# Kernel tuning notes

Hardware: AMD Instinct MI355X
Metric: run time of the kernel (lower is better)

Reference implementation:

```python
import jax, jax.numpy as jnp
import numpy as np

N_NODES = 100000
N_EDGES = 1200000
D_FEAT = 64
THETA = (1.0, -0.8, 0.4, -0.1)  # polynomial coefficients, k = len(THETA)


def setup_inputs() -> dict:
    key = jax.random.key(0)
    k1, k2, k3 = jax.random.split(key, 3)
    feat = jax.random.normal(k1, (N_NODES, D_FEAT), dtype=jnp.float32)
    src = jax.random.randint(k2, (N_EDGES,), 0, N_NODES, dtype=jnp.int32)
    dst = jax.random.randint(k3, (N_EDGES,), 0, N_NODES, dtype=jnp.int32)
    return {"feat": feat, "src": src, "dst": dst}


def reference(feat, src, dst):
    # in-degrees: number of incoming edges per node (clamped to >= 1)
    deg = jax.ops.segment_sum(jnp.ones((N_EDGES,), feat.dtype), dst, num_segments=N_NODES)
    d_invsqrt = jnp.clip(deg, 1.0, None) ** -0.5  # [N]
    d = d_invsqrt[:, None]  # [N, 1]

    h = THETA[0] * feat
    for k in range(1, len(THETA)):
        # unnLaplacian: feat - D^{-1/2} A^T (D^{-1/2} feat)  (copy_u / sum over edges)
        msg = (feat * d)[src]                                   # [E, F] gather
        agg = jax.ops.segment_sum(msg, dst, num_segments=N_NODES)  # [N, F] scatter-add
        feat = feat - agg * d
        h = h + THETA[k] * feat
    return h
```

## Files before the change

### kernel.cpp

```cpp
#include <hip/hip_runtime.h>

#define D_FEAT 64
#define BSHIFT 8
#define MAXB 512
#define CHUNK 4096

typedef float nfloat4 __attribute__((ext_vector_type(4)));

__device__ inline unsigned short f2bf(float f) {
    unsigned u = __float_as_uint(f);
    unsigned r = u + 0x7fffu + ((u >> 16) & 1u);
    return (unsigned short)(r >> 16);
}
__device__ inline float bflo(unsigned w) { return __uint_as_float(w << 16); }
__device__ inline float bfhi(unsigned w) { return __uint_as_float(w & 0xffff0000u); }

__device__ inline void unpack8(uint4 u, float* v) {
    v[0] = bflo(u.x); v[1] = bfhi(u.x);
    v[2] = bflo(u.y); v[3] = bfhi(u.y);
    v[4] = bflo(u.z); v[5] = bfhi(u.z);
    v[6] = bflo(u.w); v[7] = bfhi(u.w);
}
__device__ inline uint4 pack8(const float* v) {
    uint4 u;
    u.x = (unsigned)f2bf(v[0]) | ((unsigned)f2bf(v[1]) << 16);
    u.y = (unsigned)f2bf(v[2]) | ((unsigned)f2bf(v[3]) << 16);
    u.z = (unsigned)f2bf(v[4]) | ((unsigned)f2bf(v[5]) << 16);
    u.w = (unsigned)f2bf(v[6]) | ((unsigned)f2bf(v[7]) << 16);
    return u;
}

__global__ void pre_kernel(const int* __restrict__ dst, int* __restrict__ mat,
                           const float4* __restrict__ f, uint4* __restrict__ fb,
                           int nE, int P, int nblk, int n8) {
    __shared__ int lh[MAXB];
    int b = blockIdx.x;
    if (b < nblk) {
        for (int i = threadIdx.x; i < P; i += blockDim.x) lh[i] = 0;
        __syncthreads();
        int s = b * CHUNK;
        int e1 = s + CHUNK; if (e1 > nE) e1 = nE;
        for (int e = s + threadIdx.x; e < e1; e += blockDim.x)
            atomicAdd(&lh[dst[e] >> BSHIFT], 1);
        __syncthreads();
        for (int i = threadIdx.x; i < P; i += blockDim.x)
            mat[i * nblk + b] = lh[i];
    } else {
        int i = (b - nblk) * 256 + threadIdx.x;
        if (i < n8) {
            float4 a = f[(size_t)i * 2];
            float4 c = f[(size_t)i * 2 + 1];
            float v[8] = {a.x, a.y, a.z, a.w, c.x, c.y, c.z, c.w};
            fb[i] = pack8(v);
        }
    }
}

__global__ void scan1_kernel(const int* __restrict__ in, int* __restrict__ out,
                             int* __restrict__ bsums, int n) {
    __shared__ int tmp[256];
    int tid = threadIdx.x;
    int i = blockIdx.x * 256 + tid;
    int v = (i < n) ? in[i] : 0;
    tmp[tid] = v;
    __syncthreads();
    for (int off = 1; off < 256; off <<= 1) {
        int t2 = 0;
        if (tid >= off) t2 = tmp[tid - off];
        __syncthreads();
        tmp[tid] += t2;
        __syncthreads();
    }
    if (i < n) out[i] = tmp[tid] - v;
    if (tid == 255) bsums[blockIdx.x] = tmp[255];
}

__global__ void scan2_kernel(int* __restrict__ bsums, int nb) {
    __shared__ int tmp[512];
    int tid = threadIdx.x;
    int v = (tid < nb) ? bsums[tid] : 0;
    tmp[tid] = v;
    __syncthreads();
    for (int off = 1; off < 512; off <<= 1) {
        int t2 = 0;
        if (tid >= off) t2 = tmp[tid - off];
        __syncthreads();
        tmp[tid] += t2;
        __syncthreads();
    }
    if (tid < nb) bsums[tid] = tmp[tid] - v;
}

__global__ void scan3add_kernel(int* __restrict__ matS, const int* __restrict__ bsums,
                                int* __restrict__ bucket_ptr, int n, int nblk,
                                int P, int nE) {
    int i = blockIdx.x * 256 + threadIdx.x;
    if (i < n) {
        int v = matS[i] + bsums[blockIdx.x];
        matS[i] = v;
        if (i % nblk == 0) bucket_ptr[i / nblk] = v;
    }
    if (i == 0) bucket_ptr[P] = nE;
}

__global__ void scatter_part_kernel(const int* __restrict__ src, const int* __restrict__ dst,
                                    const int* __restrict__ matS, unsigned* __restrict__ part,
                                    int nE, int P, int nblk) {
    __shared__ int cur[MAXB];
    for (int i = threadIdx.x; i < P; i += blockDim.x)
        cur[i] = matS[i * nblk + blockIdx.x];
    __syncthreads();
    int s = blockIdx.x * CHUNK;
    int e1 = s + CHUNK; if (e1 > nE) e1 = nE;
    for (int e = s + threadIdx.x; e < e1; e += blockDim.x) {
        int t = dst[e];
        int pos = atomicAdd(&cur[t >> BSHIFT], 1);
        part[pos] = ((unsigned)src[e] << 8) | (unsigned)(t & 255);
    }
}

__global__ void bucket_csr_kernel(const unsigned* __restrict__ part,
                                  const int* __restrict__ bucket_ptr,
                                  int* __restrict__ row_ptr, int* __restrict__ row_end,
                                  float* __restrict__ dv, int* __restrict__ esrc, int nN) {
    __shared__ int hist[256];
    __shared__ int cur[256];
    __shared__ int scanT[256];
    int b = blockIdx.x;
    int tid = threadIdx.x;
    int bp0 = bucket_ptr[b], bp1 = bucket_ptr[b + 1];
    hist[tid] = 0;
    __syncthreads();
    for (int e = bp0 + tid; e < bp1; e += 256)
        atomicAdd(&hist[part[e] & 255u], 1);
    __syncthreads();
    int v = hist[tid];
    scanT[tid] = v;
    __syncthreads();
    for (int off = 1; off < 256; off <<= 1) {
        int t2 = 0;
        if (tid >= off) t2 = scanT[tid - off];
        __syncthreads();
        scanT[tid] += t2;
        __syncthreads();
    }
    int startv = scanT[tid] - v;
    cur[tid] = startv;
    int node = (b << BSHIFT) + tid;
    if (node < nN) {
        float fc = (float)(v < 1 ? 1 : v);
        dv[node] = rsqrtf(fc);
        row_ptr[node] = bp0 + startv;
        row_end[node] = bp0 + startv + v;
    }
    __syncthreads();
    for (int e = bp0 + tid; e < bp1; e += 256) {
        unsigned p = part[e];
        int rank = atomicAdd(&cur[p & 255u], 1);
        esrc[bp0 + rank] = (int)(p >> 8);
    }
}

__global__ void poly_kernel(const uint4* __restrict__ fb_in, uint4* __restrict__ fb_out,
                            const int* __restrict__ row_ptr, const int* __restrict__ row_end,
                            const int* __restrict__ esrc, const float* __restrict__ d,
                            const uint4* __restrict__ fb0, const uint4* __restrict__ fb1,
                            float* __restrict__ h, int final_step, int nN) {
    int wave = (blockIdx.x * blockDim.x + threadIdx.x) >> 6;
    int lane = threadIdx.x & 63;
    int sub  = lane >> 3;
    int q    = lane & 7;
    int t    = wave * 8 + sub;
    bool valid = (t < nN);
    if (!valid) t = nN - 1;

    int r0 = row_ptr[t], r1 = row_end[t];
    if (!valid) r1 = r0;

    float acc[8];
#pragma unroll
    for (int c = 0; c < 8; ++c) acc[c] = 0.0f;

    int   sq = 0;
    float dq = 0.0f;
    if (r0 < r1) {
        int jc = r0 + q; if (jc > r1 - 1) jc = r1 - 1;
        sq = esrc[jc];
        dq = d[sq];
    }
    int j0 = r0;
    while (j0 < r1) {
        int jn = j0 + 8;
        int   sq_n = 0;
        float dq_n = 0.0f;
        if (jn < r1) {
            int jc = jn + q; if (jc > r1 - 1) jc = r1 - 1;
            sq_n = esrc[jc];
            dq_n = d[sq_n];
        }
        int m = r1 - j0; if (m > 8) m = 8;
#pragma unroll
        for (int u = 0; u < 4; ++u) {
            int bl = (sub << 3) + u;
            int   sb = __shfl(sq, bl, 64);
            float ds = __shfl(dq, bl, 64);
            ds = (u < m) ? ds : 0.0f;
            uint4 fv = fb_in[(size_t)sb * 8 + q];
            float v[8];
            unpack8(fv, v);
#pragma unroll
            for (int c = 0; c < 8; ++c) acc[c] = fmaf(v[c], ds, acc[c]);
        }
        if (m > 4) {
#pragma unroll
            for (int u = 4; u < 8; ++u) {
                int bl = (sub << 3) + u;
                int   sb = __shfl(sq, bl, 64);
                float ds = __shfl(dq, bl, 64);
                ds = (u < m) ? ds : 0.0f;
                uint4 fv = fb_in[(size_t)sb * 8 + q];
                float v[8];
                unpack8(fv, v);
#pragma unroll
                for (int c = 0; c < 8; ++c) acc[c] = fmaf(v[c], ds, acc[c]);
            }
        }
        sq = sq_n; dq = dq_n; j0 = jn;
    }

    if (!valid) return;
    size_t idx = (size_t)t * 8 + q;
    float dt = d[t];
    float fo[8];
    unpack8(fb_in[idx], fo);
    float fn[8];
#pragma unroll
    for (int c = 0; c < 8; ++c) fn[c] = fo[c] - acc[c] * dt;

    if (!final_step) {
        fb_out[idx] = pack8(fn);
    } else {
        float f1v[8];
        unpack8(fb1[idx], f1v);
        float f0v[8];
        unpack8(fb0[idx], f0v);
        float hv[8];
#pragma unroll
        for (int c = 0; c < 8; ++c)
            hv[c] = f0v[c] - 0.8f * f1v[c] + 0.4f * fo[c] - 0.1f * fn[c];
        nfloat4 h0 = {hv[0], hv[1], hv[2], hv[3]};
        nfloat4 h1 = {hv[4], hv[5], hv[6], hv[7]};
        nfloat4* hp = (nfloat4*)(h + (size_t)t * 64 + q * 8);
        __builtin_nontemporal_store(h0, hp);
        __builtin_nontemporal_store(h1, hp + 1);
    }
}

extern "C" void kernel_launch(void* const* d_in, const int* in_sizes, int n_in,
                              void* d_out, int out_size, void* d_ws, size_t ws_size,
                              hipStream_t stream) {
    const float* feat = (const float*)d_in[0];
    const int*   src  = (const int*)d_in[1];
    const int*   dst  = (const int*)d_in[2];
    float*       h    = (float*)d_out;

    const int nN = in_sizes[0] / D_FEAT;
    const int nE = in_sizes[1];

    const int P    = (nN + 255) >> 8;
    const int nblk = (nE + CHUNK - 1) / CHUNK;
    const int n    = P * nblk;
    const int nb   = (n + 255) / 256;

    auto align = [](size_t x) { return (x + 255) & ~(size_t)255; };
    char* ws = (char*)d_ws;
    size_t off = 0;
    int*      mat        = (int*)(ws + off);      off += align((size_t)n * 4);
    int*      matS       = (int*)(ws + off);      off += align((size_t)n * 4);
    int*      bsums      = (int*)(ws + off);      off += align(512 * 4);
    int*      bucket_ptr = (int*)(ws + off);      off += align((size_t)(P + 1) * 4);
    int*      row_ptr    = (int*)(ws + off);      off += align((size_t)nN * 4);
    int*      row_end    = (int*)(ws + off);      off += align((size_t)nN * 4);
    float*    dv         = (float*)(ws + off);    off += align((size_t)nN * 4);
    unsigned* part       = (unsigned*)(ws + off); off += align((size_t)nE * 4);
    int*      esrc       = (int*)(ws + off);      off += align((size_t)nE * 4);
    size_t fbBytes = (size_t)nN * D_FEAT * 2;
    uint4*    fb0        = (uint4*)(ws + off);    off += align(fbBytes);
    uint4*    fb1        = (uint4*)(ws + off);    off += align(fbBytes);
    uint4*    fb2;
    if (ws_size >= off + fbBytes) {
        fb2 = (uint4*)(ws + off);
    } else {
        fb2 = (uint4*)d_in[0];
    }

    const int n8 = nN * 8;
    const int tb = (n8 + 255) / 256;
    pre_kernel         <<<nblk + tb, 256, 0, stream>>>(dst, mat, (const float4*)feat,
                                                       fb0, nE, P, nblk, n8);
    scan1_kernel       <<<nb, 256, 0, stream>>>(mat, matS, bsums, n);
    scan2_kernel       <<<1, 512, 0, stream>>>(bsums, nb);
    scan3add_kernel    <<<nb, 256, 0, stream>>>(matS, bsums, bucket_ptr, n, nblk, P, nE);
    scatter_part_kernel<<<nblk, 256, 0, stream>>>(src, dst, matS, part, nE, P, nblk);
    bucket_csr_kernel  <<<P, 256, 0, stream>>>(part, bucket_ptr, row_ptr, row_end,
                                               dv, esrc, nN);

    long long waves = ((long long)nN + 7) / 8;
    int polyBlocks = (int)((waves * 64 + 255) / 256);
    poly_kernel<<<polyBlocks, 256, 0, stream>>>(fb0, fb1, row_ptr, row_end, esrc, dv,
                                                nullptr, nullptr, nullptr, 0, nN);
    poly_kernel<<<polyBlocks, 256, 0, stream>>>(fb1, fb2, row_ptr, row_end, esrc, dv,
                                                nullptr, nullptr, nullptr, 0, nN);
    poly_kernel<<<polyBlocks, 256, 0, stream>>>(fb2, nullptr, row_ptr, row_end, esrc, dv,
                                                fb0, fb1, h, 1, nN);
}
```

Before: 204.8 us.

## Replace per-block bucket count matrix scan with global atomic bucket cursors

Drops the P×nblk count matrix and its three-pass prefix scan. Per-block histograms are now added atomically into per-bucket totals, a single block scans those totals, and each scatter block reserves its slice of every bucket with one global atomicAdd per nonzero bucket. Scatter blocks keep their src/dst values in registers so each edge is read once, and row_end is removed in favor of reading row_ptr[t+1]. This saves two kernel launches and the matrix traffic, at the cost of a memset, global atomic contention, and an edge order inside each bucket that is no longer deterministic.

```diff
diff --git a/kernel.cpp b/kernel.cpp
--- a/kernel.cpp
+++ b/kernel.cpp
@@ -30,7 +30,7 @@
     return u;
 }
 
-__global__ void pre_kernel(const int* __restrict__ dst, int* __restrict__ mat,
+__global__ void pre_kernel(const int* __restrict__ dst, int* __restrict__ bucket_tot,
                            const float4* __restrict__ f, uint4* __restrict__ fb,
                            int nE, int P, int nblk, int n8) {
     __shared__ int lh[MAXB];
@@ -43,8 +43,10 @@
         for (int e = s + threadIdx.x; e < e1; e += blockDim.x)
             atomicAdd(&lh[dst[e] >> BSHIFT], 1);
         __syncthreads();
-        for (int i = threadIdx.x; i < P; i += blockDim.x)
-            mat[i * nblk + b] = lh[i];
+        for (int i = threadIdx.x; i < P; i += blockDim.x) {
+            int c = lh[i];
+            if (c) atomicAdd(&bucket_tot[i], c);
+        }
     } else {
         int i = (b - nblk) * 256 + threadIdx.x;
         if (i < n8) {
@@ -56,29 +58,12 @@
     }
 }
 
-__global__ void scan1_kernel(const int* __restrict__ in, int* __restrict__ out,
-                             int* __restrict__ bsums, int n) {
-    __shared__ int tmp[256];
-    int tid = threadIdx.x;
-    int i = blockIdx.x * 256 + tid;
-    int v = (i < n) ? in[i] : 0;
-    tmp[tid] = v;
-    __syncthreads();
-    for (int off = 1; off < 256; off <<= 1) {
-        int t2 = 0;
-        if (tid >= off) t2 = tmp[tid - off];
-        __syncthreads();
-        tmp[tid] += t2;
-        __syncthreads();
-    }
-    if (i < n) out[i] = tmp[tid] - v;
-    if (tid == 255) bsums[blockIdx.x] = tmp[255];
-}
-
-__global__ void scan2_kernel(int* __restrict__ bsums, int nb) {
+__global__ void bscan_kernel(const int* __restrict__ bucket_tot, int* __restrict__ bucket_ptr,
+                             int* __restrict__ cursor, int* __restrict__ row_ptr,
+                             int P, int nE, int nN) {
     __shared__ int tmp[512];
     int tid = threadIdx.x;
-    int v = (tid < nb) ? bsums[tid] : 0;
+    int v = (tid < P) ? bucket_tot[tid] : 0;
     tmp[tid] = v;
     __syncthreads();
     for (int off = 1; off < 512; off <<= 1) {
@@ -88,40 +73,56 @@
         tmp[tid] += t2;
         __syncthreads();
     }
-    if (tid < nb) bsums[tid] = tmp[tid] - v;
-}
-
-__global__ void scan3add_kernel(int* __restrict__ matS, const int* __restrict__ bsums,
-                                int* __restrict__ bucket_ptr, int n, int nblk,
-                                int P, int nE) {
-    int i = blockIdx.x * 256 + threadIdx.x;
-    if (i < n) {
-        int v = matS[i] + bsums[blockIdx.x];
-        matS[i] = v;
-        if (i % nblk == 0) bucket_ptr[i / nblk] = v;
-    }
-    if (i == 0) bucket_ptr[P] = nE;
+    if (tid < P) {
+        int start = tmp[tid] - v;
+        bucket_ptr[tid] = start;
+        cursor[tid] = start;
+    }
+    if (tid == 0) {
+        bucket_ptr[P] = nE;
+        row_ptr[nN] = nE;
+    }
 }
 
 __global__ void scatter_part_kernel(const int* __restrict__ src, const int* __restrict__ dst,
-                                    const int* __restrict__ matS, unsigned* __restrict__ part,
-                                    int nE, int P, int nblk) {
+                                    int* __restrict__ cursor, unsigned* __restrict__ part,
+                                    int nE, int P) {
+    __shared__ int cnt[MAXB];
     __shared__ int cur[MAXB];
-    for (int i = threadIdx.x; i < P; i += blockDim.x)
-        cur[i] = matS[i * nblk + blockIdx.x];
+    for (int i = threadIdx.x; i < P; i += blockDim.x) cnt[i] = 0;
     __syncthreads();
     int s = blockIdx.x * CHUNK;
     int e1 = s + CHUNK; if (e1 > nE) e1 = nE;
-    for (int e = s + threadIdx.x; e < e1; e += blockDim.x) {
-        int t = dst[e];
-        int pos = atomicAdd(&cur[t >> BSHIFT], 1);
-        part[pos] = ((unsigned)src[e] << 8) | (unsigned)(t & 255);
+    int se[16], te[16];
+#pragma unroll
+    for (int k = 0; k < 16; ++k) {
+        int e = s + k * 256 + threadIdx.x;
+        if (e < e1) {
+            se[k] = src[e];
+            te[k] = dst[e];
+            atomicAdd(&cnt[te[k] >> BSHIFT], 1);
+        } else {
+            te[k] = -1;
+        }
+    }
+    __syncthreads();
+    for (int i = threadIdx.x; i < P; i += blockDim.x) {
+        int c = cnt[i];
+        cur[i] = c ? atomicAdd(&cursor[i], c) : 0;
+    }
+    __syncthreads();
+#pragma unroll
+    for (int k = 0; k < 16; ++k) {
+        if (te[k] >= 0) {
+            int pos = atomicAdd(&cur[te[k] >> BSHIFT], 1);
+            part[pos] = ((unsigned)se[k] << 8) | (unsigned)(te[k] & 255);
+        }
     }
 }
 
 __global__ void bucket_csr_kernel(const unsigned* __restrict__ part,
                                   const int* __restrict__ bucket_ptr,
-                                  int* __restrict__ row_ptr, int* __restrict__ row_end,
+                                  int* __restrict__ row_ptr,
                                   float* __restrict__ dv, int* __restrict__ esrc, int nN) {
     __shared__ int hist[256];
     __shared__ int cur[256];
@@ -151,7 +152,6 @@
         float fc = (float)(v < 1 ? 1 : v);
         dv[node] = rsqrtf(fc);
         row_ptr[node] = bp0 + startv;
-        row_end[node] = bp0 + startv + v;
     }
     __syncthreads();
     for (int e = bp0 + tid; e < bp1; e += 256) {
@@ -162,7 +162,7 @@
 }
 
 __global__ void poly_kernel(const uint4* __restrict__ fb_in, uint4* __restrict__ fb_out,
-                            const int* __restrict__ row_ptr, const int* __restrict__ row_end,
+                            const int* __restrict__ row_ptr,
                             const int* __restrict__ esrc, const float* __restrict__ d,
                             const uint4* __restrict__ fb0, const uint4* __restrict__ fb1,
                             float* __restrict__ h, int final_step, int nN) {
@@ -174,7 +174,7 @@
     bool valid = (t < nN);
     if (!valid) t = nN - 1;
 
-    int r0 = row_ptr[t], r1 = row_end[t];
+    int r0 = row_ptr[t], r1 = row_ptr[t + 1];
     if (!valid) r1 = r0;
 
     float acc[8];
@@ -269,18 +269,14 @@
 
     const int P    = (nN + 255) >> 8;
     const int nblk = (nE + CHUNK - 1) / CHUNK;
-    const int n    = P * nblk;
-    const int nb   = (n + 255) / 256;
 
     auto align = [](size_t x) { return (x + 255) & ~(size_t)255; };
     char* ws = (char*)d_ws;
     size_t off = 0;
-    int*      mat        = (int*)(ws + off);      off += align((size_t)n * 4);
-    int*      matS       = (int*)(ws + off);      off += align((size_t)n * 4);
-    int*      bsums      = (int*)(ws + off);      off += align(512 * 4);
+    int*      bucket_tot = (int*)(ws + off);      off += align((size_t)P * 4);
     int*      bucket_ptr = (int*)(ws + off);      off += align((size_t)(P + 1) * 4);
-    int*      row_ptr    = (int*)(ws + off);      off += align((size_t)nN * 4);
-    int*      row_end    = (int*)(ws + off);      off += align((size_t)nN * 4);
+    int*      cursor     = (int*)(ws + off);      off += align((size_t)P * 4);
+    int*      row_ptr    = (int*)(ws + off);      off += align((size_t)(nN + 1) * 4);
     float*    dv         = (float*)(ws + off);    off += align((size_t)nN * 4);
     unsigned* part       = (unsigned*)(ws + off); off += align((size_t)nE * 4);
     int*      esrc       = (int*)(ws + off);      off += align((size_t)nE * 4);
@@ -296,21 +292,21 @@
 
     const int n8 = nN * 8;
     const int tb = (n8 + 255) / 256;
-    pre_kernel         <<<nblk + tb, 256, 0, stream>>>(dst, mat, (const float4*)feat,
+
+    hipMemsetAsync(bucket_tot, 0, (size_t)P * 4, stream);
+    pre_kernel         <<<nblk + tb, 256, 0, stream>>>(dst, bucket_tot, (const float4*)feat,
                                                        fb0, nE, P, nblk, n8);
-    scan1_kernel       <<<nb, 256, 0, stream>>>(mat, matS, bsums, n);
-    scan2_kernel       <<<1, 512, 0, stream>>>(bsums, nb);
-    scan3add_kernel    <<<nb, 256, 0, stream>>>(matS, bsums, bucket_ptr, n, nblk, P, nE);
-    scatter_part_kernel<<<nblk, 256, 0, stream>>>(src, dst, matS, part, nE, P, nblk);
-    bucket_csr_kernel  <<<P, 256, 0, stream>>>(part, bucket_ptr, row_ptr, row_end,
-                                               dv, esrc, nN);
+    bscan_kernel       <<<1, 512, 0, stream>>>(bucket_tot, bucket_ptr, cursor, row_ptr,
+                                               P, nE, nN);
+    scatter_part_kernel<<<nblk, 256, 0, stream>>>(src, dst, cursor, part, nE, P);
+    bucket_csr_kernel  <<<P, 256, 0, stream>>>(part, bucket_ptr, row_ptr, dv, esrc, nN);
 
     long long waves = ((long long)nN + 7) / 8;
     int polyBlocks = (int)((waves * 64 + 255) / 256);
-    poly_kernel<<<polyBlocks, 256, 0, stream>>>(fb0, fb1, row_ptr, row_end, esrc, dv,
+    poly_kernel<<<polyBlocks, 256, 0, stream>>>(fb0, fb1, row_ptr, esrc, dv,
                                                 nullptr, nullptr, nullptr, 0, nN);
-    poly_kernel<<<polyBlocks, 256, 0, stream>>>(fb1, fb2, row_ptr, row_end, esrc, dv,
+    poly_kernel<<<polyBlocks, 256, 0, stream>>>(fb1, fb2, row_ptr, esrc, dv,
                                                 nullptr, nullptr, nullptr, 0, nN);
-    poly_kernel<<<polyBlocks, 256, 0, stream>>>(fb2, nullptr, row_ptr, row_end, esrc, dv,
+    poly_kernel<<<polyBlocks, 256, 0, stream>>>(fb2, nullptr, row_ptr, esrc, dv,
                                                 fb0, fb1, h, 1, nN);
 }
```

Measured after the change: 209.8 us. 2.4% more time.
